# Kernel tuning notes

Hardware: AMD Instinct MI355X
Metric: run time of the kernel (lower is better)

Reference implementation:

```python
import jax, jax.numpy as jnp
import numpy as np

# NSA hyperparams (match init_kwargs)
D_BLK = 64    # d: block stride
L_CMP = 64    # compression block length (== d -> non-overlapping blocks)
L_SLC = 64    # selection block length (== l_cmp == d -> P_slc = P_cmp)
BQ = 64       # block_size_q
TOPK = 16     # slc_top_k
WL, WR = 512, 0  # sliding window (left, right)


def _nsa_forward(q, k, v, w_k, b_k, w_v, b_v, w_gate, b_gate, seqlen):
    S, qh, dim = q.shape
    kv = k.shape[1]
    H = qh // kv
    b = S // seqlen          # number of equal-length packed sequences
    s = seqlen
    scale = dim ** -0.5
    f32 = jnp.float32

    # [b, s, kv, H, e]: q head g*H+h belongs to kv head g (repeat_interleave layout)
    q5 = q.reshape(b, s, kv, H, dim)
    k3 = k.reshape(b, s, kv, dim)
    v3 = v.reshape(b, s, kv, dim)

    # ---- block compression (extract_blocks + cmp_linear over block length) ----
    n_blk = s // D_BLK
    kb = k.reshape(b, n_blk, D_BLK, kv, dim)
    vb = v.reshape(b, n_blk, D_BLK, kv, dim)
    K_cmp = jnp.einsum('bntke,t->bnke', kb, w_k) + b_k[0]
    V_cmp = jnp.einsum('bntke,t->bnke', vb, w_v) + b_v[0]

    # ---- compressed attention (per sequence, fp32 softmax) ----
    sc = jnp.einsum('bqkhe,bnke->bkhqn', q5, K_cmp).astype(f32) * scale
    P = jax.nn.softmax(sc, axis=-1)
    out_cmp = jnp.einsum('bkhqn,bnke->bqkhe', P.astype(q.dtype), V_cmp)

    # ---- selection scores: pool P over q-blocks and GQA groups, then top-k ----
    nqb = s // BQ
    pooled = P.reshape(b, kv, H, nqb, BQ, n_blk).sum(axis=(2, 4))  # [b,kv,nqb,n_blk]
    idx = jax.lax.top_k(pooled, TOPK)[1]                            # [b,kv,nqb,TOPK]

    # gather selected K/V blocks (shared by all queries in a q-block / GQA group)
    kb2 = jnp.transpose(kb, (0, 3, 1, 2, 4))  # [b,kv,n_blk,l,e]
    vb2 = jnp.transpose(vb, (0, 3, 1, 2, 4))
    gather = jax.vmap(jax.vmap(lambda blocks, i: blocks[i]))
    K_sel = gather(kb2, idx)  # [b,kv,nqb,TOPK,l,e]
    V_sel = gather(vb2, idx)

    # ---- selected-block attention ----
    qblk = q5.reshape(b, nqb, BQ, kv, H, dim)
    sc2 = jnp.einsum('bnckhe,bkntle->bkhnctl', qblk, K_sel).astype(f32) * scale
    sc2 = sc2.reshape(b, kv, H, nqb, BQ, TOPK * L_SLC)
    P2 = jax.nn.softmax(sc2, axis=-1).astype(q.dtype)
    out_slc = jnp.einsum('bkhncm,bknme->bnckhe', P2,
                         V_sel.reshape(b, kv, nqb, TOPK * L_SLC, dim))
    out_slc = out_slc.reshape(b, s, kv, H, dim)

    # ---- sliding-window attention (window_size=(WL, WR), non-causal flag) ----
    sw = jnp.einsum('bikhe,bjke->bkhij', q5, k3).astype(f32) * scale
    i = jnp.arange(s)[:, None]
    j = jnp.arange(s)[None, :]
    valid = (j >= i - WL) & (j <= i + WR)
    sw = jnp.where(valid, sw, -jnp.inf)
    Pw = jax.nn.softmax(sw, axis=-1).astype(q.dtype)
    out_win = jnp.einsum('bkhij,bjke->bikhe', Pw, v3)

    # ---- gated fusion of the three branches ----
    gate = jax.nn.sigmoid(jnp.einsum('bqkhe,ec->bqkhc', q5, w_gate) + b_gate)
    out = (gate[..., 0:1] * out_cmp
           + gate[..., 1:2] * out_slc
           + gate[..., 2:3] * out_win)
    return out.reshape(S, qh, dim)


def setup_inputs() -> dict:
    key = jax.random.key(0)
    ks = jax.random.split(key, 9)
    S, qh, kvh, dim = 4096, 8, 2, 128
    inp = {
        'q': jax.random.normal(ks[0], (S, qh, dim), jnp.float32),
        'k': jax.random.normal(ks[1], (S, kvh, dim), jnp.float32),
        'v': jax.random.normal(ks[2], (S, kvh, dim), jnp.float32),
        'w_k': jax.random.normal(ks[3], (L_CMP,), jnp.float32) * (L_CMP ** -0.5),
        'b_k': jax.random.normal(ks[4], (1,), jnp.float32) * 0.02,
        'w_v': jax.random.normal(ks[5], (L_CMP,), jnp.float32) * (L_CMP ** -0.5),
        'b_v': jax.random.normal(ks[6], (1,), jnp.float32) * 0.02,
        'w_gate': jax.random.normal(ks[7], (dim, 3), jnp.float32) * (dim ** -0.5),
        'b_gate': jax.random.normal(ks[8], (3,), jnp.float32) * 0.02,
        'seqlen': 2048,
    }
    return inp


def reference(q, k, v, w_k, b_k, w_v, b_v, w_gate, b_gate, seqlen):
    return _nsa_forward(q, k, v, w_k, b_k, w_v, b_v, w_gate, b_gate, seqlen)
```

## Files before the change

### kernel.cpp

```cpp
#include <hip/hip_runtime.h>
#include <hip/hip_bf16.h>


#define SEQ   2048
#define NB    2
#define KV    2
#define NH    4
#define QH    8
#define DIM   128
#define NBLK  32
#define NQB   32
#define NTOP  16
#define SCALE 0.08838834764831845f
#define QS    36
#define RS    144
#define VP    72

typedef unsigned short ushort_t;
using bf16x8 = __attribute__((ext_vector_type(8))) short;
using f32x4  = __attribute__((ext_vector_type(4))) float;

__device__ __forceinline__ unsigned pkbf(float a, float b){
  union { __hip_bfloat162 h; unsigned u; } cv;
  cv.h = __float22bfloat162_rn(make_float2(a, b));
  return cv.u;
}

__device__ __forceinline__ void async16(ushort_t* l, const ushort_t* g){
  __builtin_amdgcn_global_load_lds(
      (const __attribute__((address_space(1))) unsigned int*)(size_t)g,
      (__attribute__((address_space(3))) unsigned int*)(size_t)l,
      16, 0, 0);
}

__global__ __launch_bounds__(256) void prep_k(
    const float* __restrict__ k, const float* __restrict__ v,
    ushort_t* __restrict__ Kb, ushort_t* __restrict__ VT)
{
  int blk = blockIdx.x;
  int db = blk & 1, rb = (blk >> 1) & 31, bbg = blk >> 6;
  int bb = bbg >> 1, g = bbg & 1;
  int tid = threadIdx.x;
  __shared__ ushort_t T[64*VP];

  for (int jj = 0; jj < 4; ++jj){
    int i = tid + jj*256;
    int r = i >> 4, ds = i & 15;
    size_t src = ((size_t)(bb*SEQ + rb*64 + r)*KV + g)*DIM + db*64 + ds*4;
    float4 kx = *(const float4*)(k + src);
    float4 vx = *(const float4*)(v + src);
    uint2 kk; kk.x = pkbf(kx.x,kx.y); kk.y = pkbf(kx.z,kx.w);
    size_t rowb = ((size_t)bbg*SEQ + rb*64 + r)*DIM*2;
    int swz = (db*128 + ds*8) ^ ((r & 7) << 4);
    *(uint2*)((char*)Kb + rowb + swz) = kk;
    unsigned v01 = pkbf(vx.x,vx.y), v23 = pkbf(vx.z,vx.w);
    T[(ds*4+0)*VP + r] = (ushort_t)(v01 & 0xffffu);
    T[(ds*4+1)*VP + r] = (ushort_t)(v01 >> 16);
    T[(ds*4+2)*VP + r] = (ushort_t)(v23 & 0xffffu);
    T[(ds*4+3)*VP + r] = (ushort_t)(v23 >> 16);
  }
  __syncthreads();
  for (int jj = 0; jj < 4; ++jj){
    int i = tid + jj*256;
    int d = i >> 4, seg = i & 15;
    uint2 u = *(uint2*)&T[d*VP + seg*4];
    size_t rowb = ((size_t)bbg*DIM + db*64 + d)*SEQ*2;
    int swz = (seg*8) ^ ((d & 7) << 4);
    *(uint2*)((char*)VT + rowb + rb*128 + swz) = u;
  }
}

__global__ __launch_bounds__(256) void compress_k(
    const float* __restrict__ k, const float* __restrict__ v,
    const float* __restrict__ w_k, const float* __restrict__ b_k,
    const float* __restrict__ w_v, const float* __restrict__ b_v,
    float* __restrict__ Kc, float* __restrict__ Vc)
{
  int blk = blockIdx.x;
  int dh = blk & 1;
  int n  = (blk >> 1) & 31;
  int g  = (blk >> 6) & 1;
  int bb = blk >> 7;
  int tid = threadIdx.x;

  __shared__ float wks[64], wvs[64];
  __shared__ float accK[16][64], accV[16][64];
  if (tid < 64){ wks[tid] = w_k[tid]; wvs[tid] = w_v[tid]; }
  __syncthreads();

  int r4 = tid >> 4, dq = tid & 15;
  float4 sk = {0,0,0,0}, sv = {0,0,0,0};
  for (int rr = 0; rr < 4; ++rr){
    int row = r4*4 + rr;
    size_t off = ((size_t)(bb*SEQ + n*64 + row)*KV + g)*DIM + dh*64 + dq*4;
    float4 kx = *(const float4*)(k + off);
    float4 vx = *(const float4*)(v + off);
    float a = wks[row], b = wvs[row];
    sk.x += a*kx.x; sk.y += a*kx.y; sk.z += a*kx.z; sk.w += a*kx.w;
    sv.x += b*vx.x; sv.y += b*vx.y; sv.z += b*vx.z; sv.w += b*vx.w;
  }
  *(float4*)&accK[r4][dq*4] = sk;
  *(float4*)&accV[r4][dq*4] = sv;
  __syncthreads();
  size_t obase = ((size_t)((bb*KV+g)*NBLK + n))*DIM + dh*64;
  if (tid < 64){
    float s = 0.f;
#pragma unroll
    for (int i = 0; i < 16; ++i) s += accK[i][tid];
    Kc[obase + tid] = s + b_k[0];
  } else if (tid < 128){
    int d = tid - 64;
    float s = 0.f;
#pragma unroll
    for (int i = 0; i < 16; ++i) s += accV[i][d];
    Vc[obase + d] = s + b_v[0];
  }
}

__global__ __launch_bounds__(256) void cmp_attn_k(
    const float* __restrict__ q, const float* __restrict__ Kc,
    const float* __restrict__ Vc,
    const float* __restrict__ w_gate, const float* __restrict__ b_gate,
    float* __restrict__ pooled_part, float* __restrict__ out)
{
  int blk = blockIdx.x;
  int h  = blk & 3;
  int qb = (blk >> 2) & (NQB-1);
  int g  = (blk >> 7) & 1;
  int bb = blk >> 8;
  int tid = threadIdx.x;
  int qi = tid >> 2, c = tid & 3;

  __shared__ float Ks[32*RS];
  __shared__ float Vs[32*RS];
  __shared__ float wsum[4][NBLK];

  const float4* Ksrc = (const float4*)(Kc + (size_t)(bb*KV + g) * NBLK * DIM);
  const float4* Vsrc = (const float4*)(Vc + (size_t)(bb*KV + g) * NBLK * DIM);
  for (int i = tid; i < 1024; i += 256){
    int row = i >> 5, seg = i & 31;
    int dst = row*RS + (seg>>3)*QS + (seg&7)*4;
    ((float4*)(Ks+dst))[0] = Ksrc[i];
    ((float4*)(Vs+dst))[0] = Vsrc[i];
  }
  __syncthreads();

  int row = bb*SEQ + qb*64 + qi;
  float qv[32];
  {
    const float4* q4 = (const float4*)(q + ((size_t)row*QH + g*NH + h)*DIM + c*32);
#pragma unroll
    for (int j = 0; j < 8; ++j){
      float4 u = q4[j];
      qv[4*j+0]=u.x; qv[4*j+1]=u.y; qv[4*j+2]=u.z; qv[4*j+3]=u.w;
    }
  }

  float gp = 0.f;
#pragma unroll
  for (int d = 0; d < 32; ++d) gp += qv[d]*w_gate[(c*32+d)*3 + 0];
  gp += __shfl_xor(gp, 1); gp += __shfl_xor(gp, 2);
  float g0 = 1.f/(1.f + expf(-(gp + b_gate[0])));

  float sc[NBLK];
#pragma unroll
  for (int n = 0; n < NBLK; ++n){
    float p = 0.f;
    const float4* kr = (const float4*)(Ks + n*RS + c*QS);
#pragma unroll
    for (int j = 0; j < 8; ++j){
      float4 u = kr[j];
      p += qv[4*j+0]*u.x + qv[4*j+1]*u.y + qv[4*j+2]*u.z + qv[4*j+3]*u.w;
    }
    p += __shfl_xor(p, 1); p += __shfl_xor(p, 2);
    sc[n] = p * SCALE;
  }
  float m = sc[0];
#pragma unroll
  for (int n = 1; n < NBLK; ++n) m = fmaxf(m, sc[n]);
  float l = 0.f;
#pragma unroll
  for (int n = 0; n < NBLK; ++n){ sc[n] = expf(sc[n]-m); l += sc[n]; }
  float inv = 1.f/l;
#pragma unroll
  for (int n = 0; n < NBLK; ++n) sc[n] *= inv;

#pragma unroll
  for (int n = 0; n < NBLK; ++n){
    float t2 = sc[n];
    t2 += __shfl_xor(t2, 4); t2 += __shfl_xor(t2, 8);
    t2 += __shfl_xor(t2, 16); t2 += __shfl_xor(t2, 32);
    if ((tid & 63) == 0) wsum[tid>>6][n] = t2;
  }
  __syncthreads();
  if (tid < NBLK)
    pooled_part[(size_t)blk*NBLK + tid] =
        (wsum[0][tid]+wsum[1][tid]) + (wsum[2][tid]+wsum[3][tid]);

  float o[32];
#pragma unroll
  for (int d = 0; d < 32; ++d) o[d] = 0.f;
#pragma unroll
  for (int n = 0; n < NBLK; ++n){
    float pb = sc[n];
    const float4* vr = (const float4*)(Vs + n*RS + c*QS);
#pragma unroll
    for (int j = 0; j < 8; ++j){
      float4 u = vr[j];
      o[4*j+0] += pb*u.x; o[4*j+1] += pb*u.y;
      o[4*j+2] += pb*u.z; o[4*j+3] += pb*u.w;
    }
  }
  float* op = out + ((size_t)row*QH + g*NH + h)*DIM + c*32;
#pragma unroll
  for (int d = 0; d < 32; ++d) op[d] = g0*o[d];
}

__global__ __launch_bounds__(256, 2) void attn_k(
    const float* __restrict__ q, const ushort_t* __restrict__ Kb,
    const ushort_t* __restrict__ VT, const float* __restrict__ pp,
    const float* __restrict__ w_gate, const float* __restrict__ b_gate,
    float* __restrict__ slcbuf, float* __restrict__ out)
{
  int idx = blockIdx.x;
  int x = idx & 7, low = idx & 1, u = idx >> 3;
  int bbg = x >> 1;
  int j = u*2 + low;
  int role = j >> 7;
  int qb = (j >> 2) & 31;
  int h  = j & 3;
  int bb = bbg >> 1, g = bbg & 1;

  int tid = threadIdx.x;
  int lane = tid & 63, w = tid >> 6, quad = lane >> 4, l15 = lane & 15;
  int xr = (l15 & 7) << 4;

  __shared__ ushort_t Ks[2][64*128];
  __shared__ ushort_t VTs[2][128*64];
  __shared__ ushort_t Ps[64*VP];
  __shared__ float gbuf[64];
  __shared__ int   idxs[NTOP];

  if (role == 0 && tid < 64){
    int n = lane;
    float val = -INFINITY;
    if (n < NBLK){
      const float* p0 = pp + ((size_t)((bb*KV+g)*NQB + qb)*NH)*NBLK + n;
      val = (p0[0] + p0[NBLK]) + (p0[2*NBLK] + p0[3*NBLK]);
    }
    for (int t = 0; t < NTOP; ++t){
      float bv = val; int bi = n;
      for (int mm = 1; mm < 32; mm <<= 1){
        float ov = __shfl_xor(bv, mm);
        int   oi = __shfl_xor(bi, mm);
        if (ov > bv || (ov == bv && oi < bi)){ bv = ov; bi = oi; }
      }
      if (lane == 0) idxs[t] = bi;
      if (n == bi) val = -INFINITY;
    }
  }

  const float* qrow = q + ((size_t)(bb*SEQ + qb*64 + w*16 + l15)*QH + g*NH + h)*DIM;
  int gcol = 1 + role;
  bf16x8 qfrag[4];
  float gp = 0.f;
#pragma unroll
  for (int kc = 0; kc < 4; ++kc){
    int d0 = kc*32 + quad*8;
    float4 u0 = *(const float4*)(qrow + d0);
    float4 u1 = *(const float4*)(qrow + d0 + 4);
    float qf[8] = {u0.x,u0.y,u0.z,u0.w,u1.x,u1.y,u1.z,u1.w};
#pragma unroll
    for (int jj = 0; jj < 8; ++jj) gp += qf[jj]*w_gate[(d0+jj)*3 + gcol];
    union { unsigned uu[4]; bf16x8 v8; } tq;
    tq.uu[0] = pkbf(u0.x,u0.y); tq.uu[1] = pkbf(u0.z,u0.w);
    tq.uu[2] = pkbf(u1.x,u1.y); tq.uu[3] = pkbf(u1.z,u1.w);
    qfrag[kc] = tq.v8;
  }
  gp += __shfl_xor(gp,16); gp += __shfl_xor(gp,32);
  if (quad == 0) gbuf[w*16+l15] = 1.f/(1.f + __expf(-(gp + b_gate[gcol])));
  __syncthreads();
  float gl[4];
#pragma unroll
  for (int r = 0; r < 4; ++r) gl[r] = gbuf[w*16+quad*4+r];

  const ushort_t* kbase  = Kb + (size_t)bbg*SEQ*DIM;
  const ushort_t* vtbase = VT + (size_t)bbg*DIM*SEQ;

  int kb0 = (qb >= 8) ? (qb - 8) : 0;
  int nph = (role == 0) ? NTOP : (qb - kb0 + 1);
  int qi_local = w*16 + l15;

  float m1 = -INFINITY, l1 = 0.f;
  f32x4 oacc[8];
  const f32x4 zero4 = {0.f,0.f,0.f,0.f};
#pragma unroll
  for (int dt = 0; dt < 8; ++dt) oacc[dt] = zero4;

  auto stage = [&](int bufi, int kb_){
    const ushort_t* ksrc = kbase + (size_t)kb_*64*DIM;
#pragma unroll
    for (int jj = 0; jj < 4; ++jj){
      int i = tid + jj*256;
      async16(&Ks[bufi][(jj*256 + w*64)*8], ksrc + (size_t)i*8);
    }
    const ushort_t* vsrc = vtbase + kb_*64;
#pragma unroll
    for (int jj = 0; jj < 4; ++jj){
      int i = tid + jj*256;
      int d = i >> 3, sg = i & 7;
      async16(&VTs[bufi][(jj*256 + w*64)*8], vsrc + (size_t)d*SEQ + sg*8);
    }
  };

  stage(0, (role == 0) ? idxs[0] : kb0);

  for (int t = 0; t < nph; ++t){
    int cur = t & 1;
    int kb = (role == 0) ? idxs[t] : (kb0 + t);
    __syncthreads();
    if (t+1 < nph){
      int kbn = (role == 0) ? idxs[t+1] : (kb0 + t + 1);
      stage(cur ^ 1, kbn);
    }
    __builtin_amdgcn_sched_barrier(0);

    f32x4 sacc[4];
#pragma unroll
    for (int nt = 0; nt < 4; ++nt) sacc[nt] = zero4;
    __builtin_amdgcn_s_setprio(1);
#pragma unroll
    for (int kc = 0; kc < 4; ++kc){
      bf16x8 b = qfrag[kc];
#pragma unroll
      for (int nt = 0; nt < 4; ++nt){
        bf16x8 a = *(bf16x8*)((char*)&Ks[cur][0] + (nt*16 + l15)*256
                              + ((kc*64 + quad*16) ^ xr));
        sacc[nt] = __builtin_amdgcn_mfma_f32_16x16x32_bf16(a, b, sacc[nt], 0, 0, 0);
      }
    }
    __builtin_amdgcn_s_setprio(0);

    bool mlow  = (role == 1) && (kb == qb - 8);
    bool mhigh = (role == 1) && (kb == qb);
    float mx = -INFINITY;
    if (mlow | mhigh){
#pragma unroll
      for (int nt = 0; nt < 4; ++nt)
#pragma unroll
        for (int r = 0; r < 4; ++r){
          int key = nt*16 + quad*4 + r;
          float sv = sacc[nt][r]*SCALE;
          bool valid = (!mlow || key >= qi_local) && (!mhigh || key <= qi_local);
          sv = valid ? sv : -INFINITY;
          sacc[nt][r] = sv;
          mx = fmaxf(mx, sv);
        }
    } else {
#pragma unroll
      for (int nt = 0; nt < 4; ++nt)
#pragma unroll
        for (int r = 0; r < 4; ++r){
          float sv = sacc[nt][r]*SCALE;
          sacc[nt][r] = sv;
          mx = fmaxf(mx, sv);
        }
    }
    mx = fmaxf(mx, __shfl_xor(mx, 16));
    mx = fmaxf(mx, __shfl_xor(mx, 32));
    float mn = fmaxf(m1, mx);
    float al = __expf(m1 - mn);
    float s0 = 0.f;
#pragma unroll
    for (int nt = 0; nt < 4; ++nt)
#pragma unroll
      for (int r = 0; r < 4; ++r){
        float pe = __expf(sacc[nt][r] - mn);
        sacc[nt][r] = pe;
        s0 += pe;
      }
    s0 += __shfl_xor(s0, 16);
    s0 += __shfl_xor(s0, 32);
    l1 = l1*al + s0;
    m1 = mn;

#pragma unroll
    for (int nt = 0; nt < 4; ++nt){
      uint2 pk;
      pk.x = pkbf(sacc[nt][0], sacc[nt][1]);
      pk.y = pkbf(sacc[nt][2], sacc[nt][3]);
      *(uint2*)&Ps[(w*16 + l15)*VP + nt*16 + quad*4] = pk;
    }

    float ar[4];
#pragma unroll
    for (int r = 0; r < 4; ++r) ar[r] = __shfl(al, quad*4 + r);
#pragma unroll
    for (int dt = 0; dt < 8; ++dt)
#pragma unroll
      for (int r = 0; r < 4; ++r) oacc[dt][r] *= ar[r];
#pragma unroll
    for (int kc2 = 0; kc2 < 2; ++kc2){
      bf16x8 pa = *(bf16x8*)&Ps[(w*16 + l15)*VP + kc2*32 + quad*8];
      __builtin_amdgcn_s_setprio(1);
#pragma unroll
      for (int dt = 0; dt < 8; ++dt){
        bf16x8 vb8 = *(bf16x8*)((char*)&VTs[cur][0] + (dt*16 + l15)*128
                                + ((kc2*64 + quad*16) ^ xr));
        oacc[dt] = __builtin_amdgcn_mfma_f32_16x16x32_bf16(pa, vb8, oacc[dt], 0, 0, 0);
      }
      __builtin_amdgcn_s_setprio(0);
    }
  }

  float lr[4];
#pragma unroll
  for (int r = 0; r < 4; ++r) lr[r] = __shfl(l1, quad*4 + r);
#pragma unroll
  for (int r = 0; r < 4; ++r){
    float s2 = gl[r] / lr[r];
    size_t ob = ((size_t)(bb*SEQ + qb*64 + w*16 + quad*4 + r)*QH + g*NH + h)*DIM + l15;
    if (role == 0){
      float* op = slcbuf + ob;
#pragma unroll
      for (int dt = 0; dt < 8; ++dt) op[dt*16] = s2 * oacc[dt][r];
    } else {
      float* op = out + ob;
#pragma unroll
      for (int dt = 0; dt < 8; ++dt) op[dt*16] += s2 * oacc[dt][r];
    }
  }
}

__global__ __launch_bounds__(256) void merge_k(const float* __restrict__ slcbuf,
                                               float* __restrict__ out){
  int i = blockIdx.x * 256 + threadIdx.x;
  float4 a = ((const float4*)slcbuf)[i];
  float4 b = ((float4*)out)[i];
  b.x += a.x; b.y += a.y; b.z += a.z; b.w += a.w;
  ((float4*)out)[i] = b;
}

extern "C" void kernel_launch(void* const* d_in, const int* in_sizes, int n_in,
                              void* d_out, int out_size, void* d_ws, size_t ws_size,
                              hipStream_t stream) {
  const float* q      = (const float*)d_in[0];
  const float* k      = (const float*)d_in[1];
  const float* v      = (const float*)d_in[2];
  const float* w_k    = (const float*)d_in[3];
  const float* b_k    = (const float*)d_in[4];
  const float* w_v    = (const float*)d_in[5];
  const float* b_v    = (const float*)d_in[6];
  const float* w_gate = (const float*)d_in[7];
  const float* b_gate = (const float*)d_in[8];
  float* out = (float*)d_out;

  float* ws     = (float*)d_ws;
  float* Kc     = ws;
  float* Vc     = ws + 16384;
  float* pp     = ws + 32768;
  float* slcbuf = ws + 49152;
  ushort_t* Kb  = (ushort_t*)(ws + 4243456);
  ushort_t* VT  = Kb + 1048576;

  prep_k    <<<256, 256, 0, stream>>>(k, v, Kb, VT);
  compress_k<<<256, 256, 0, stream>>>(k, v, w_k, b_k, w_v, b_v, Kc, Vc);
  cmp_attn_k<<<NB*KV*NQB*NH, 256, 0, stream>>>(q, Kc, Vc, w_gate, b_gate, pp, out);
  attn_k    <<<1024, 256, 0, stream>>>(q, Kb, VT, pp, w_gate, b_gate, slcbuf, out);
  merge_k   <<<4096, 256, 0, stream>>>(slcbuf, out);
}
```

Baseline: 186.4 us.

## Process all four GQA heads per block to share staged K/V tiles

Each attn_k workgroup now has 8 waves covering all four query heads of a KV group for one q-block, with each wave handling two 16-row query tiles. The selected or windowed K/V blocks are loaded into LDS once and reused by all heads, cutting global-to-LDS traffic by four and halving the grid to 256 blocks of 512 threads. Q is pre-scaled by scale·log2(e) so the softmax can use exp2f. A lazy rescale skips the output correction when the running max grows by at most 8. The cost is more registers and LDS per block, fewer blocks in flight, and a small precision risk from the lazy max.

```diff
diff --git a/kernel.cpp b/kernel.cpp
--- a/kernel.cpp
+++ b/kernel.cpp
@@ -12,6 +12,7 @@
 #define NQB   32
 #define NTOP  16
 #define SCALE 0.08838834764831845f
+#define QSC   0.12751831795244785f
 #define QS    36
 #define RS    144
 #define VP    72
@@ -216,7 +217,7 @@
   for (int d = 0; d < 32; ++d) op[d] = g0*o[d];
 }
 
-__global__ __launch_bounds__(256, 2) void attn_k(
+__global__ __launch_bounds__(512, 2) void attn_k(
     const float* __restrict__ q, const ushort_t* __restrict__ Kb,
     const ushort_t* __restrict__ VT, const float* __restrict__ pp,
     const float* __restrict__ w_gate, const float* __restrict__ b_gate,
@@ -226,19 +227,20 @@
   int x = idx & 7, low = idx & 1, u = idx >> 3;
   int bbg = x >> 1;
   int j = u*2 + low;
-  int role = j >> 7;
-  int qb = (j >> 2) & 31;
-  int h  = j & 3;
+  int role = j >> 5;
+  int qb = j & 31;
   int bb = bbg >> 1, g = bbg & 1;
 
   int tid = threadIdx.x;
-  int lane = tid & 63, w = tid >> 6, quad = lane >> 4, l15 = lane & 15;
+  int lane = tid & 63, w = tid >> 6;
+  int quad = lane >> 4, l15 = lane & 15;
+  int h = w & 3, qh2 = w >> 2;
   int xr = (l15 & 7) << 4;
 
   __shared__ ushort_t Ks[2][64*128];
   __shared__ ushort_t VTs[2][128*64];
-  __shared__ ushort_t Ps[64*VP];
-  __shared__ float gbuf[64];
+  __shared__ ushort_t Ps[256*VP];
+  __shared__ float gbuf[256];
   __shared__ int   idxs[NTOP];
 
   if (role == 0 && tid < 64){
@@ -260,56 +262,71 @@
     }
   }
 
-  const float* qrow = q + ((size_t)(bb*SEQ + qb*64 + w*16 + l15)*QH + g*NH + h)*DIM;
+  const float* qrow0 = q + ((size_t)(bb*SEQ + qb*64 + qh2*32 + l15)*QH + g*NH + h)*DIM;
+  const float* qrow1 = qrow0 + (size_t)16*QH*DIM;
   int gcol = 1 + role;
-  bf16x8 qfrag[4];
-  float gp = 0.f;
+  bf16x8 qfrag0[4], qfrag1[4];
+  float gp0 = 0.f, gp1 = 0.f;
 #pragma unroll
   for (int kc = 0; kc < 4; ++kc){
     int d0 = kc*32 + quad*8;
-    float4 u0 = *(const float4*)(qrow + d0);
-    float4 u1 = *(const float4*)(qrow + d0 + 4);
-    float qf[8] = {u0.x,u0.y,u0.z,u0.w,u1.x,u1.y,u1.z,u1.w};
-#pragma unroll
-    for (int jj = 0; jj < 8; ++jj) gp += qf[jj]*w_gate[(d0+jj)*3 + gcol];
-    union { unsigned uu[4]; bf16x8 v8; } tq;
-    tq.uu[0] = pkbf(u0.x,u0.y); tq.uu[1] = pkbf(u0.z,u0.w);
-    tq.uu[2] = pkbf(u1.x,u1.y); tq.uu[3] = pkbf(u1.z,u1.w);
-    qfrag[kc] = tq.v8;
-  }
-  gp += __shfl_xor(gp,16); gp += __shfl_xor(gp,32);
-  if (quad == 0) gbuf[w*16+l15] = 1.f/(1.f + __expf(-(gp + b_gate[gcol])));
+    float4 a0 = *(const float4*)(qrow0 + d0);
+    float4 a1 = *(const float4*)(qrow0 + d0 + 4);
+    float4 b0 = *(const float4*)(qrow1 + d0);
+    float4 b1 = *(const float4*)(qrow1 + d0 + 4);
+    float qa[8] = {a0.x,a0.y,a0.z,a0.w,a1.x,a1.y,a1.z,a1.w};
+    float qc[8] = {b0.x,b0.y,b0.z,b0.w,b1.x,b1.y,b1.z,b1.w};
+#pragma unroll
+    for (int jj = 0; jj < 8; ++jj){
+      float wg = w_gate[(d0+jj)*3 + gcol];
+      gp0 += qa[jj]*wg; gp1 += qc[jj]*wg;
+    }
+    union { unsigned uu[4]; bf16x8 v8; } t0, t1;
+#pragma unroll
+    for (int p2 = 0; p2 < 4; ++p2){
+      t0.uu[p2] = pkbf(qa[2*p2]*QSC, qa[2*p2+1]*QSC);
+      t1.uu[p2] = pkbf(qc[2*p2]*QSC, qc[2*p2+1]*QSC);
+    }
+    qfrag0[kc] = t0.v8; qfrag1[kc] = t1.v8;
+  }
+  gp0 += __shfl_xor(gp0,16); gp0 += __shfl_xor(gp0,32);
+  gp1 += __shfl_xor(gp1,16); gp1 += __shfl_xor(gp1,32);
+  if (quad == 0){
+    gbuf[w*32 + l15]      = 1.f/(1.f + __expf(-(gp0 + b_gate[gcol])));
+    gbuf[w*32 + 16 + l15] = 1.f/(1.f + __expf(-(gp1 + b_gate[gcol])));
+  }
   __syncthreads();
-  float gl[4];
-#pragma unroll
-  for (int r = 0; r < 4; ++r) gl[r] = gbuf[w*16+quad*4+r];
+  float gl0[4], gl1[4];
+#pragma unroll
+  for (int r = 0; r < 4; ++r){
+    gl0[r] = gbuf[w*32 + quad*4 + r];
+    gl1[r] = gbuf[w*32 + 16 + quad*4 + r];
+  }
 
   const ushort_t* kbase  = Kb + (size_t)bbg*SEQ*DIM;
   const ushort_t* vtbase = VT + (size_t)bbg*DIM*SEQ;
 
   int kb0 = (qb >= 8) ? (qb - 8) : 0;
   int nph = (role == 0) ? NTOP : (qb - kb0 + 1);
-  int qi_local = w*16 + l15;
-
-  float m1 = -INFINITY, l1 = 0.f;
-  f32x4 oacc[8];
+  int qi0 = qh2*32 + l15, qi1 = qi0 + 16;
+
+  float m10 = -INFINITY, l10 = 0.f, m11 = -INFINITY, l11 = 0.f;
+  f32x4 oacc0[8], oacc1[8];
   const f32x4 zero4 = {0.f,0.f,0.f,0.f};
 #pragma unroll
-  for (int dt = 0; dt < 8; ++dt) oacc[dt] = zero4;
+  for (int dt = 0; dt < 8; ++dt){ oacc0[dt] = zero4; oacc1[dt] = zero4; }
 
   auto stage = [&](int bufi, int kb_){
     const ushort_t* ksrc = kbase + (size_t)kb_*64*DIM;
 #pragma unroll
-    for (int jj = 0; jj < 4; ++jj){
-      int i = tid + jj*256;
-      async16(&Ks[bufi][(jj*256 + w*64)*8], ksrc + (size_t)i*8);
-    }
+    for (int jj = 0; jj < 2; ++jj)
+      async16(&Ks[bufi][(jj*512 + w*64)*8], ksrc + (size_t)(tid + jj*512)*8);
     const ushort_t* vsrc = vtbase + kb_*64;
 #pragma unroll
-    for (int jj = 0; jj < 4; ++jj){
-      int i = tid + jj*256;
+    for (int jj = 0; jj < 2; ++jj){
+      int i = tid + jj*512;
       int d = i >> 3, sg = i & 7;
-      async16(&VTs[bufi][(jj*256 + w*64)*8], vsrc + (size_t)d*SEQ + sg*8);
+      async16(&VTs[bufi][(jj*512 + w*64)*8], vsrc + (size_t)d*SEQ + sg*8);
     }
   };
 
@@ -325,109 +342,148 @@
     }
     __builtin_amdgcn_sched_barrier(0);
 
-    f32x4 sacc[4];
-#pragma unroll
-    for (int nt = 0; nt < 4; ++nt) sacc[nt] = zero4;
+    f32x4 sacc0[4], sacc1[4];
+#pragma unroll
+    for (int nt = 0; nt < 4; ++nt){ sacc0[nt] = zero4; sacc1[nt] = zero4; }
     __builtin_amdgcn_s_setprio(1);
 #pragma unroll
     for (int kc = 0; kc < 4; ++kc){
-      bf16x8 b = qfrag[kc];
 #pragma unroll
       for (int nt = 0; nt < 4; ++nt){
         bf16x8 a = *(bf16x8*)((char*)&Ks[cur][0] + (nt*16 + l15)*256
                               + ((kc*64 + quad*16) ^ xr));
-        sacc[nt] = __builtin_amdgcn_mfma_f32_16x16x32_bf16(a, b, sacc[nt], 0, 0, 0);
+        sacc0[nt] = __builtin_amdgcn_mfma_f32_16x16x32_bf16(a, qfrag0[kc], sacc0[nt], 0, 0, 0);
+        sacc1[nt] = __builtin_amdgcn_mfma_f32_16x16x32_bf16(a, qfrag1[kc], sacc1[nt], 0, 0, 0);
       }
     }
     __builtin_amdgcn_s_setprio(0);
 
     bool mlow  = (role == 1) && (kb == qb - 8);
     bool mhigh = (role == 1) && (kb == qb);
-    float mx = -INFINITY;
-    if (mlow | mhigh){
+    bool domask = mlow | mhigh;
+
+    auto softmax_qt = [&](f32x4* sc, float& m1r, float& l1r, int qi_l,
+                          bool& skipped) -> float {
+      float mx = -INFINITY;
+      if (domask){
+#pragma unroll
+        for (int nt = 0; nt < 4; ++nt)
+#pragma unroll
+          for (int r = 0; r < 4; ++r){
+            int key = nt*16 + quad*4 + r;
+            float sv = sc[nt][r];
+            bool valid = (!mlow || key >= qi_l) && (!mhigh || key <= qi_l);
+            sv = valid ? sv : -INFINITY;
+            sc[nt][r] = sv;
+            mx = fmaxf(mx, sv);
+          }
+      } else {
+#pragma unroll
+        for (int nt = 0; nt < 4; ++nt)
+#pragma unroll
+          for (int r = 0; r < 4; ++r) mx = fmaxf(mx, sc[nt][r]);
+      }
+      mx = fmaxf(mx, __shfl_xor(mx, 16));
+      mx = fmaxf(mx, __shfl_xor(mx, 32));
+      float al = 1.f;
+      skipped = __all(mx <= m1r + 8.f);
+      if (!skipped){
+        float mn = fmaxf(m1r, mx);
+        al = exp2f(m1r - mn);
+        m1r = mn;
+      }
+      float s0 = 0.f;
 #pragma unroll
       for (int nt = 0; nt < 4; ++nt)
 #pragma unroll
         for (int r = 0; r < 4; ++r){
-          int key = nt*16 + quad*4 + r;
-          float sv = sacc[nt][r]*SCALE;
-          bool valid = (!mlow || key >= qi_local) && (!mhigh || key <= qi_local);
-          sv = valid ? sv : -INFINITY;
-          sacc[nt][r] = sv;
-          mx = fmaxf(mx, sv);
+          float pe = exp2f(sc[nt][r] - m1r);
+          sc[nt][r] = pe;
+          s0 += pe;
         }
-    } else {
-#pragma unroll
-      for (int nt = 0; nt < 4; ++nt)
-#pragma unroll
-        for (int r = 0; r < 4; ++r){
-          float sv = sacc[nt][r]*SCALE;
-          sacc[nt][r] = sv;
-          mx = fmaxf(mx, sv);
-        }
-    }
-    mx = fmaxf(mx, __shfl_xor(mx, 16));
-    mx = fmaxf(mx, __shfl_xor(mx, 32));
-    float mn = fmaxf(m1, mx);
-    float al = __expf(m1 - mn);
-    float s0 = 0.f;
-#pragma unroll
-    for (int nt = 0; nt < 4; ++nt)
-#pragma unroll
-      for (int r = 0; r < 4; ++r){
-        float pe = __expf(sacc[nt][r] - mn);
-        sacc[nt][r] = pe;
-        s0 += pe;
-      }
-    s0 += __shfl_xor(s0, 16);
-    s0 += __shfl_xor(s0, 32);
-    l1 = l1*al + s0;
-    m1 = mn;
+      s0 += __shfl_xor(s0, 16);
+      s0 += __shfl_xor(s0, 32);
+      l1r = l1r*al + s0;
+      return al;
+    };
+    bool sk0, sk1;
+    float al0 = softmax_qt(sacc0, m10, l10, qi0, sk0);
+    float al1 = softmax_qt(sacc1, m11, l11, qi1, sk1);
 
 #pragma unroll
     for (int nt = 0; nt < 4; ++nt){
-      uint2 pk;
-      pk.x = pkbf(sacc[nt][0], sacc[nt][1]);
-      pk.y = pkbf(sacc[nt][2], sacc[nt][3]);
-      *(uint2*)&Ps[(w*16 + l15)*VP + nt*16 + quad*4] = pk;
-    }
-
-    float ar[4];
-#pragma unroll
-    for (int r = 0; r < 4; ++r) ar[r] = __shfl(al, quad*4 + r);
-#pragma unroll
-    for (int dt = 0; dt < 8; ++dt)
-#pragma unroll
-      for (int r = 0; r < 4; ++r) oacc[dt][r] *= ar[r];
+      uint2 p0, p1;
+      p0.x = pkbf(sacc0[nt][0], sacc0[nt][1]);
+      p0.y = pkbf(sacc0[nt][2], sacc0[nt][3]);
+      p1.x = pkbf(sacc1[nt][0], sacc1[nt][1]);
+      p1.y = pkbf(sacc1[nt][2], sacc1[nt][3]);
+      *(uint2*)&Ps[(w*32 + l15)*VP + nt*16 + quad*4] = p0;
+      *(uint2*)&Ps[(w*32 + 16 + l15)*VP + nt*16 + quad*4] = p1;
+    }
+
+    if (!sk0){
+      float ar[4];
+#pragma unroll
+      for (int r = 0; r < 4; ++r) ar[r] = __shfl(al0, quad*4 + r);
+#pragma unroll
+      for (int dt = 0; dt < 8; ++dt)
+#pragma unroll
+        for (int r = 0; r < 4; ++r) oacc0[dt][r] *= ar[r];
+    }
+    if (!sk1){
+      float ar[4];
+#pragma unroll
+      for (int r = 0; r < 4; ++r) ar[r] = __shfl(al1, quad*4 + r);
+#pragma unroll
+      for (int dt = 0; dt < 8; ++dt)
+#pragma unroll
+        for (int r = 0; r < 4; ++r) oacc1[dt][r] *= ar[r];
+    }
+
 #pragma unroll
     for (int kc2 = 0; kc2 < 2; ++kc2){
-      bf16x8 pa = *(bf16x8*)&Ps[(w*16 + l15)*VP + kc2*32 + quad*8];
+      bf16x8 pa0 = *(bf16x8*)&Ps[(w*32 + l15)*VP + kc2*32 + quad*8];
+      bf16x8 pa1 = *(bf16x8*)&Ps[(w*32 + 16 + l15)*VP + kc2*32 + quad*8];
       __builtin_amdgcn_s_setprio(1);
 #pragma unroll
       for (int dt = 0; dt < 8; ++dt){
         bf16x8 vb8 = *(bf16x8*)((char*)&VTs[cur][0] + (dt*16 + l15)*128
                                 + ((kc2*64 + quad*16) ^ xr));
-        oacc[dt] = __builtin_amdgcn_mfma_f32_16x16x32_bf16(pa, vb8, oacc[dt], 0, 0, 0);
+        oacc0[dt] = __builtin_amdgcn_mfma_f32_16x16x32_bf16(pa0, vb8, oacc0[dt], 0, 0, 0);
+        oacc1[dt] = __builtin_amdgcn_mfma_f32_16x16x32_bf16(pa1, vb8, oacc1[dt], 0, 0, 0);
       }
       __builtin_amdgcn_s_setprio(0);
     }
   }
 
-  float lr[4];
-#pragma unroll
-  for (int r = 0; r < 4; ++r) lr[r] = __shfl(l1, quad*4 + r);
+  float lr0[4], lr1[4];
 #pragma unroll
   for (int r = 0; r < 4; ++r){
-    float s2 = gl[r] / lr[r];
-    size_t ob = ((size_t)(bb*SEQ + qb*64 + w*16 + quad*4 + r)*QH + g*NH + h)*DIM + l15;
+    lr0[r] = __shfl(l10, quad*4 + r);
+    lr1[r] = __shfl(l11, quad*4 + r);
+  }
+#pragma unroll
+  for (int r = 0; r < 4; ++r){
+    float s20 = gl0[r] / lr0[r];
+    float s21 = gl1[r] / lr1[r];
+    size_t ob0 = ((size_t)(bb*SEQ + qb*64 + qh2*32 + quad*4 + r)*QH + g*NH + h)*DIM + l15;
+    size_t ob1 = ob0 + (size_t)16*QH*DIM;
     if (role == 0){
-      float* op = slcbuf + ob;
-#pragma unroll
-      for (int dt = 0; dt < 8; ++dt) op[dt*16] = s2 * oacc[dt][r];
+      float* op0 = slcbuf + ob0;
+      float* op1 = slcbuf + ob1;
+#pragma unroll
+      for (int dt = 0; dt < 8; ++dt){
+        op0[dt*16] = s20 * oacc0[dt][r];
+        op1[dt*16] = s21 * oacc1[dt][r];
+      }
     } else {
-      float* op = out + ob;
-#pragma unroll
-      for (int dt = 0; dt < 8; ++dt) op[dt*16] += s2 * oacc[dt][r];
+      float* op0 = out + ob0;
+      float* op1 = out + ob1;
+#pragma unroll
+      for (int dt = 0; dt < 8; ++dt){
+        op0[dt*16] += s20 * oacc0[dt][r];
+        op1[dt*16] += s21 * oacc1[dt][r];
+      }
     }
   }
 }
@@ -466,6 +522,6 @@
   prep_k    <<<256, 256, 0, stream>>>(k, v, Kb, VT);
   compress_k<<<256, 256, 0, stream>>>(k, v, w_k, b_k, w_v, b_v, Kc, Vc);
   cmp_attn_k<<<NB*KV*NQB*NH, 256, 0, stream>>>(q, Kc, Vc, w_gate, b_gate, pp, out);
-  attn_k    <<<1024, 256, 0, stream>>>(q, Kb, VT, pp, w_gate, b_gate, slcbuf, out);
+  attn_k    <<<256, 512, 0, stream>>>(q, Kb, VT, pp, w_gate, b_gate, slcbuf, out);
   merge_k   <<<4096, 256, 0, stream>>>(slcbuf, out);
 }
```

New measurement: 186.0 us. Within noise of the previous version (-0.2%).
